# Performance work log

Hardware: AMD Instinct MI355X
Metric: run time of the kernel (lower is better)

## Reference

```python
import math
import jax, jax.numpy as jnp
import numpy as np

SAMPLE_RATE = 24000
HARMONIC_NUM = 8
SINE_AMP = 0.1


def setup_inputs() -> dict:
    key = jax.random.key(0)
    k1, k2, k3 = jax.random.split(key, 3)
    f0 = jax.random.uniform(k1, (32, 800), dtype=jnp.float32)  # frame-rate F0
    W = jax.random.normal(k2, (9, 1), dtype=jnp.float32) * (1.0 / 3.0)  # Linear(9,1) weight
    b = jax.random.normal(k3, (1,), dtype=jnp.float32) * 0.01
    return {"f0": f0, "W": W, "b": b, "upp": 240}


def reference(f0, W, b, upp):
    # nearest-neighbor upsample by integer factor upp == repeat each frame
    f0_up = jnp.repeat(f0, upp, axis=1)  # [batch, samples]
    batch, samples = f0_up.shape
    # harmonic multipliers h = 1..harmonic_num+1 (9 harmonics)
    h = jnp.arange(1, HARMONIC_NUM + 2, dtype=f0.dtype)  # [9]
    # cumsum(f0_up * h) == cumsum(f0_up) * h (cumsum is linear); one scan for all harmonics
    base_phase = jnp.cumsum(f0_up / SAMPLE_RATE, axis=1)  # [batch, samples]
    phase = base_phase[:, :, None] * (h * (2.0 * math.pi))  # [batch, samples, 9]
    sine = jnp.sin(phase) * SINE_AMP
    uv = (f0_up > 0).astype(f0.dtype)[:, :, None]  # [batch, samples, 1]
    harmonics = sine * uv
    har_source = jnp.tanh(harmonics @ W + b)  # [batch, samples, 1]
    noise = jax.random.normal(jax.random.key(1234), (batch, samples, 1), dtype=f0.dtype) * (SINE_AMP / 3.0)
    return (har_source, noise, uv)
```

## Files before the change

### kernel.cpp

```cpp
#include <hip/hip_runtime.h>
#include <stdint.h>

#define FRAMES  800
#define UPP     240
#define SAMPLES (FRAMES * UPP)
#define BATCH   32
#define NTOT    (BATCH * SAMPLES)

__device__ __forceinline__ uint32_t rotl32(uint32_t v, int d) {
  return (v << d) | (v >> (32 - d));
}

__device__ __forceinline__ void threefry2x32(uint32_t k0, uint32_t k1,
                                             uint32_t x0, uint32_t x1,
                                             uint32_t& o0, uint32_t& o1) {
  const uint32_t ks0 = k0, ks1 = k1, ks2 = k0 ^ k1 ^ 0x1BD11BDAu;
  x0 += ks0; x1 += ks1;
#define TF_R(r) { x0 += x1; x1 = rotl32(x1, r); x1 ^= x0; }
  TF_R(13) TF_R(15) TF_R(26) TF_R(6)   x0 += ks1; x1 += ks2 + 1u;
  TF_R(17) TF_R(29) TF_R(16) TF_R(24)  x0 += ks2; x1 += ks0 + 2u;
  TF_R(13) TF_R(15) TF_R(26) TF_R(6)   x0 += ks0; x1 += ks1 + 3u;
  TF_R(17) TF_R(29) TF_R(16) TF_R(24)  x0 += ks1; x1 += ks2 + 4u;
  TF_R(13) TF_R(15) TF_R(26) TF_R(6)   x0 += ks2; x1 += ks0 + 5u;
#undef TF_R
  o0 = x0; o1 = x1;
}

__device__ __forceinline__ float erfinv_f32(float x) {
  float w = -log1pf(-x * x);
  float p;
  if (w < 5.0f) {
    w = w - 2.5f;
    p = 2.81022636e-08f;
    p = fmaf(p, w, 3.43273939e-07f);
    p = fmaf(p, w, -3.5233877e-06f);
    p = fmaf(p, w, -4.39150654e-06f);
    p = fmaf(p, w, 0.00021858087f);
    p = fmaf(p, w, -0.00125372503f);
    p = fmaf(p, w, -0.00417768164f);
    p = fmaf(p, w, 0.246640727f);
    p = fmaf(p, w, 1.50140941f);
  } else {
    w = sqrtf(w) - 3.0f;
    p = -0.000200214257f;
    p = fmaf(p, w, 0.000100950558f);
    p = fmaf(p, w, 0.00134934322f);
    p = fmaf(p, w, -0.00367342844f);
    p = fmaf(p, w, 0.00573950773f);
    p = fmaf(p, w, -0.0076224613f);
    p = fmaf(p, w, 0.00943887047f);
    p = fmaf(p, w, 1.00167406f);
    p = fmaf(p, w, 2.83297682f);
  }
  return p * x;
}

__device__ __forceinline__ float bits_to_noise(uint32_t bits) {
  float f = __uint_as_float((bits >> 9) | 0x3f800000u);
  float u = f - 1.0f;
  const float lo = -0.99999994f;
  float val = fmaf(u, 2.0f, lo);
  val = fmaxf(lo, val);
  float n = 1.41421356f * erfinv_f32(val);
  return n * 0.033333335f;
}

__device__ __forceinline__ float fast_tanhf(float x) {
  float e = __expf(-2.0f * x);
  return (1.0f - e) * __builtin_amdgcn_rcpf(1.0f + e);
}

__global__ __launch_bounds__(256) void fused_kernel(
    const float* __restrict__ f0, const float* __restrict__ W,
    const float* __restrict__ bptr, float* __restrict__ out) {
  const int row = blockIdx.y;
  const float* f0row = f0 + row * FRAMES;

  const int blockSample0 = blockIdx.x * 1024;
  const int Fb = blockSample0 / UPP;

  __shared__ double sBase;
  if (threadIdx.x < 64) {
    double p = 0.0;
    for (int i = threadIdx.x; i < Fb; i += 64) p += (double)f0row[i];
#pragma unroll
    for (int off = 32; off > 0; off >>= 1) p += __shfl_xor(p, off, 64);
    if (threadIdx.x == 0) sBase = p;
  }
  __syncthreads();

  const int t0 = blockSample0 + (int)threadIdx.x * 4;
  if (t0 >= SAMPLES) return;

  const int frame = t0 / UPP;
  double prefix = sBase;
#pragma unroll
  for (int i = 0; i < 5; ++i) {
    int idx = Fb + i;
    int idxc = (idx < FRAMES - 1) ? idx : (FRAMES - 1);
    double v = (double)f0row[idxc];
    prefix += (idx < frame) ? v : 0.0;
  }
  double c = prefix * 0.01;
  const float pf = (float)(c - floor(c));

  const int j = t0 - frame * UPP;
  const float fv   = f0row[frame];
  const float step = fv * (1.0f / 24000.0f);
  const float amp  = (fv > 0.0f) ? 0.1f : 0.0f;
  const float uvf  = (fv > 0.0f) ? 1.0f : 0.0f;

  float Wr[9];
#pragma unroll
  for (int h = 0; h < 9; ++h) Wr[h] = W[h];
  const float bias = bptr[0];

  const uint32_t gbase = (uint32_t)(row * SAMPLES + t0);

  float4 hv, nv;
  float* hvp = &hv.x;
  float* nvp = &nv.x;
#pragma unroll
  for (int k = 0; k < 4; ++k) {
    float ph = fmaf((float)(j + 1 + k), step, pf);
    ph -= (ph >= 1.0f) ? 1.0f : 0.0f;
    float s1 = __builtin_amdgcn_sinf(ph);
    float c1 = __builtin_amdgcn_cosf(ph);
    float tc = 2.0f * c1;
    float skm1 = 0.0f, sk = s1;
    float dot = Wr[0] * s1;
#pragma unroll
    for (int h = 2; h <= 9; ++h) {
      float sn = tc * sk - skm1;
      skm1 = sk; sk = sn;
      dot = fmaf(Wr[h - 1], sn, dot);
    }
    hvp[k] = fast_tanhf(fmaf(amp, dot, bias));

    uint32_t a, b;
    threefry2x32(0u, 1234u, 0u, gbase + (uint32_t)k, a, b);
    nvp[k] = bits_to_noise(a ^ b);
  }

  float* har   = out;
  float* noise = out + NTOT;
  float* uvp   = out + 2 * NTOT;
  *(float4*)(har + gbase)   = hv;
  *(float4*)(noise + gbase) = nv;
  *(float4*)(uvp + gbase)   = make_float4(uvf, uvf, uvf, uvf);
}

extern "C" void kernel_launch(void* const* d_in, const int* in_sizes, int n_in,
                              void* d_out, int out_size, void* d_ws, size_t ws_size,
                              hipStream_t stream) {
  const float* f0 = (const float*)d_in[0];
  const float* W  = (const float*)d_in[1];
  const float* b  = (const float*)d_in[2];
  (void)d_ws; (void)ws_size;

  float* out = (float*)d_out;
  dim3 g((SAMPLES + 1023) / 1024, BATCH);
  fused_kernel<<<g, 256, 0, stream>>>(f0, W, b, out);
}
```

Before: 111.8 us.

## Process 8 samples per thread, share per-frame phase prefix, branchless erfinv

Each thread now handles 8 samples instead of 4, which halves the block count. The block-level f0 prefix sum is spread across all 4 waves, and per-frame phase offsets are computed once into shared memory rather than each thread redoing a 5-frame double loop. erfinv evaluates both polynomial branches and selects one, avoiding divergence, and uses hardware log and sqrt intrinsics. Phase wrap uses fract and the Chebyshev recurrence uses fma. The trade-offs are higher register pressure and fewer blocks, plus a possible small accuracy change from the hardware log.

```diff
diff --git a/kernel.cpp b/kernel.cpp
--- a/kernel.cpp
+++ b/kernel.cpp
@@ -6,6 +6,10 @@
 #define SAMPLES (FRAMES * UPP)
 #define BATCH   32
 #define NTOT    (BATCH * SAMPLES)
+#define SPT     8
+#define BLK     256
+#define SPB     (BLK * SPT)
+#define NFRM    10
 
 __device__ __forceinline__ uint32_t rotl32(uint32_t v, int d) {
   return (v << d) | (v >> (32 - d));
@@ -27,31 +31,33 @@
 }
 
 __device__ __forceinline__ float erfinv_f32(float x) {
-  float w = -log1pf(-x * x);
-  float p;
-  if (w < 5.0f) {
-    w = w - 2.5f;
-    p = 2.81022636e-08f;
-    p = fmaf(p, w, 3.43273939e-07f);
-    p = fmaf(p, w, -3.5233877e-06f);
-    p = fmaf(p, w, -4.39150654e-06f);
-    p = fmaf(p, w, 0.00021858087f);
-    p = fmaf(p, w, -0.00125372503f);
-    p = fmaf(p, w, -0.00417768164f);
-    p = fmaf(p, w, 0.246640727f);
-    p = fmaf(p, w, 1.50140941f);
-  } else {
-    w = sqrtf(w) - 3.0f;
-    p = -0.000200214257f;
-    p = fmaf(p, w, 0.000100950558f);
-    p = fmaf(p, w, 0.00134934322f);
-    p = fmaf(p, w, -0.00367342844f);
-    p = fmaf(p, w, 0.00573950773f);
-    p = fmaf(p, w, -0.0076224613f);
-    p = fmaf(p, w, 0.00943887047f);
-    p = fmaf(p, w, 1.00167406f);
-    p = fmaf(p, w, 2.83297682f);
-  }
+  float q  = __fmul_rn(x, x);
+  float om = __fsub_rn(1.0f, q);
+  float w  = -0.69314718f * __builtin_amdgcn_logf(om);
+
+  float wm = w - 2.5f;
+  float pm = 2.81022636e-08f;
+  pm = fmaf(pm, wm, 3.43273939e-07f);
+  pm = fmaf(pm, wm, -3.5233877e-06f);
+  pm = fmaf(pm, wm, -4.39150654e-06f);
+  pm = fmaf(pm, wm, 0.00021858087f);
+  pm = fmaf(pm, wm, -0.00125372503f);
+  pm = fmaf(pm, wm, -0.00417768164f);
+  pm = fmaf(pm, wm, 0.246640727f);
+  pm = fmaf(pm, wm, 1.50140941f);
+
+  float wt = __builtin_amdgcn_sqrtf(w) - 3.0f;
+  float pt = -0.000200214257f;
+  pt = fmaf(pt, wt, 0.000100950558f);
+  pt = fmaf(pt, wt, 0.00134934322f);
+  pt = fmaf(pt, wt, -0.00367342844f);
+  pt = fmaf(pt, wt, 0.00573950773f);
+  pt = fmaf(pt, wt, -0.0076224613f);
+  pt = fmaf(pt, wt, 0.00943887047f);
+  pt = fmaf(pt, wt, 1.00167406f);
+  pt = fmaf(pt, wt, 2.83297682f);
+
+  float p = (w < 5.0f) ? pm : pt;
   return p * x;
 }
 
@@ -75,35 +81,37 @@
     const float* __restrict__ bptr, float* __restrict__ out) {
   const int row = blockIdx.y;
   const float* f0row = f0 + row * FRAMES;
+  const int blockSample0 = blockIdx.x * SPB;
+  const int Fb = blockSample0 / UPP;
+  const int tid = (int)threadIdx.x;
 
-  const int blockSample0 = blockIdx.x * 1024;
-  const int Fb = blockSample0 / UPP;
+  __shared__ double sPart[4];
+  __shared__ float  sPre[NFRM];
 
-  __shared__ double sBase;
-  if (threadIdx.x < 64) {
-    double p = 0.0;
-    for (int i = threadIdx.x; i < Fb; i += 64) p += (double)f0row[i];
+  double p = 0.0;
+  for (int i = tid; i < Fb; i += BLK) p += (double)f0row[i];
 #pragma unroll
-    for (int off = 32; off > 0; off >>= 1) p += __shfl_xor(p, off, 64);
-    if (threadIdx.x == 0) sBase = p;
+  for (int off = 32; off > 0; off >>= 1) p += __shfl_xor(p, off, 64);
+  if ((tid & 63) == 0) sPart[tid >> 6] = p;
+  __syncthreads();
+
+  if (tid < NFRM) {
+    double base = (sPart[0] + sPart[1]) + (sPart[2] + sPart[3]);
+    for (int i = 0; i < tid; ++i) {
+      int idx = Fb + i;
+      idx = (idx < FRAMES) ? idx : (FRAMES - 1);
+      base += (double)f0row[idx];
+    }
+    double c = base * 0.01;
+    sPre[tid] = (float)(c - floor(c));
   }
   __syncthreads();
 
-  const int t0 = blockSample0 + (int)threadIdx.x * 4;
+  const int t0 = blockSample0 + tid * SPT;
   if (t0 >= SAMPLES) return;
 
   const int frame = t0 / UPP;
-  double prefix = sBase;
-#pragma unroll
-  for (int i = 0; i < 5; ++i) {
-    int idx = Fb + i;
-    int idxc = (idx < FRAMES - 1) ? idx : (FRAMES - 1);
-    double v = (double)f0row[idxc];
-    prefix += (idx < frame) ? v : 0.0;
-  }
-  double c = prefix * 0.01;
-  const float pf = (float)(c - floor(c));
-
+  const float pf = sPre[frame - Fb];
   const int j = t0 - frame * UPP;
   const float fv   = f0row[frame];
   const float step = fv * (1.0f / 24000.0f);
@@ -117,13 +125,12 @@
 
   const uint32_t gbase = (uint32_t)(row * SAMPLES + t0);
 
-  float4 hv, nv;
-  float* hvp = &hv.x;
-  float* nvp = &nv.x;
+  float hq[SPT], nq[SPT];
+
 #pragma unroll
-  for (int k = 0; k < 4; ++k) {
+  for (int k = 0; k < SPT; ++k) {
     float ph = fmaf((float)(j + 1 + k), step, pf);
-    ph -= (ph >= 1.0f) ? 1.0f : 0.0f;
+    ph = __builtin_amdgcn_fractf(ph);
     float s1 = __builtin_amdgcn_sinf(ph);
     float c1 = __builtin_amdgcn_cosf(ph);
     float tc = 2.0f * c1;
@@ -131,23 +138,30 @@
     float dot = Wr[0] * s1;
 #pragma unroll
     for (int h = 2; h <= 9; ++h) {
-      float sn = tc * sk - skm1;
+      float sn = fmaf(tc, sk, -skm1);
       skm1 = sk; sk = sn;
       dot = fmaf(Wr[h - 1], sn, dot);
     }
-    hvp[k] = fast_tanhf(fmaf(amp, dot, bias));
+    hq[k] = fast_tanhf(fmaf(amp, dot, bias));
+  }
 
+#pragma unroll
+  for (int k = 0; k < SPT; ++k) {
     uint32_t a, b;
     threefry2x32(0u, 1234u, 0u, gbase + (uint32_t)k, a, b);
-    nvp[k] = bits_to_noise(a ^ b);
+    nq[k] = bits_to_noise(a ^ b);
   }
 
   float* har   = out;
   float* noise = out + NTOT;
   float* uvp   = out + 2 * NTOT;
-  *(float4*)(har + gbase)   = hv;
-  *(float4*)(noise + gbase) = nv;
-  *(float4*)(uvp + gbase)   = make_float4(uvf, uvf, uvf, uvf);
+  *(float4*)(har + gbase)       = make_float4(hq[0], hq[1], hq[2], hq[3]);
+  *(float4*)(har + gbase + 4)   = make_float4(hq[4], hq[5], hq[6], hq[7]);
+  *(float4*)(noise + gbase)     = make_float4(nq[0], nq[1], nq[2], nq[3]);
+  *(float4*)(noise + gbase + 4) = make_float4(nq[4], nq[5], nq[6], nq[7]);
+  const float4 uv4 = make_float4(uvf, uvf, uvf, uvf);
+  *(float4*)(uvp + gbase)       = uv4;
+  *(float4*)(uvp + gbase + 4)   = uv4;
 }
 
 extern "C" void kernel_launch(void* const* d_in, const int* in_sizes, int n_in,
@@ -159,6 +173,6 @@
   (void)d_ws; (void)ws_size;
 
   float* out = (float*)d_out;
-  dim3 g((SAMPLES + 1023) / 1024, BATCH);
-  fused_kernel<<<g, 256, 0, stream>>>(f0, W, b, out);
+  dim3 g((SAMPLES + SPB - 1) / SPB, BATCH);
+  fused_kernel<<<g, BLK, 0, stream>>>(f0, W, b, out);
 }
```

New measurement: 102.6 us. 1.09x faster.
